# Performance work log

Measured on AMD Instinct MI355X. Metric: run time of the kernel, lower is better.

## Reference

```python
import jax, jax.numpy as jnp
import numpy as np

B, P, S, E, H, NC, NR, NL = 32, 1024, 128, 768, 8, 5, 3, 3


def _adjacency():
    adj = np.zeros((NC, NC, NR), dtype=np.float32)
    for i, j in [(0, 1), (0, 2), (1, 2), (2, 3)]:  # co-occurrence (symmetric)
        adj[i, j, 0] = 1.0
        adj[j, i, 0] = 1.0
    adj[3, 2, 1] = 1.0  # hierarchical
    for i in range(NC):  # self loops
        adj[i, i, 2] = 1.0
    return jnp.asarray(adj)


def _ln(x, g, b, eps=1e-5):
    m = x.mean(-1, keepdims=True)
    v = ((x - m) ** 2).mean(-1, keepdims=True)
    return (x - m) * jax.lax.rsqrt(v + eps) * g + b


def _mha(q, k, v, Wqkv, bqkv, Wo, bo, h=H):
    # torch nn.MultiheadAttention, batch_first=True, eval mode (no dropout),
    # returns (output, attn weights averaged over heads)
    Bq, Lq, Eq = q.shape
    Lk = k.shape[1]
    d = Eq // h
    Wq, Wk, Wv = jnp.split(Wqkv, 3, axis=0)
    bq, bk, bv = jnp.split(bqkv, 3, axis=0)
    qh = (q @ Wq.T + bq).reshape(Bq, Lq, h, d).transpose(0, 2, 1, 3)
    kh = (k @ Wk.T + bk).reshape(Bq, Lk, h, d).transpose(0, 2, 1, 3)
    vh = (v @ Wv.T + bv).reshape(Bq, Lk, h, d).transpose(0, 2, 1, 3)
    scores = jnp.einsum('bhqd,bhkd->bhqk', qh, kh) / jnp.sqrt(jnp.asarray(d, q.dtype))
    a = jax.nn.softmax(scores, axis=-1)
    o = jnp.einsum('bhqk,bhkd->bhqd', a, vh).transpose(0, 2, 1, 3).reshape(Bq, Lq, Eq)
    return o @ Wo.T + bo, a.mean(axis=1)


def setup_inputs() -> dict:
    key = jax.random.key(0)
    ks = iter(jax.random.split(key, 64))
    n = lambda *s: jax.random.normal(next(ks), s, dtype=jnp.float32) * 0.02
    return {
        'visual_features': jax.random.normal(next(ks), (B, P, E), dtype=jnp.float32),
        'text_features': jax.random.normal(next(ks), (B, S, E), dtype=jnp.float32),
        'sentence_embedding': jax.random.normal(next(ks), (B, E), dtype=jnp.float32),
        'class_presence': (jax.random.uniform(next(ks), (B, NC)) > 0.5).astype(jnp.float32),
        # graph layer params stacked over NL layers
        'g_node_emb': n(NL, NC, E), 'g_edge_emb': n(NL, NR, E),
        'g_Wqkv': n(NL, 3 * E, E), 'g_bqkv': jnp.zeros((NL, 3 * E)),
        'g_Wo': n(NL, E, E), 'g_bo': jnp.zeros((NL, E)),
        'g_W1': n(NL, E, 2 * E), 'g_b1': jnp.zeros((NL, E)),
        'g_lng': jnp.ones((NL, E)), 'g_lnb': jnp.zeros((NL, E)),
        'g_W2': n(NL, E, E), 'g_b2': jnp.zeros((NL, E)),
        # visual-text fusion MHA
        'v_Wqkv': n(3 * E, E), 'v_bqkv': jnp.zeros((3 * E,)),
        'v_Wo': n(E, E), 'v_bo': jnp.zeros((E,)),
        # per-class feature generators stacked over NC classes
        'c_W1': n(NC, E, E), 'c_b1': jnp.zeros((NC, E)),
        'c_lng': jnp.ones((NC, E)), 'c_lnb': jnp.zeros((NC, E)),
        'c_W2': n(NC, E, E), 'c_b2': jnp.zeros((NC, E)),
        # global fusion MLP
        'gf_W1': n(E, 2 * E), 'gf_b1': jnp.zeros((E,)),
        'gf_lng': jnp.ones((E,)), 'gf_lnb': jnp.zeros((E,)),
        'gf_W2': n(E, E), 'gf_b2': jnp.zeros((E,)),
        # output proj + final norm
        'out_W': n(E, E), 'out_b': jnp.zeros((E,)),
        'norm_g': jnp.ones((E,)), 'norm_b': jnp.zeros((E,)),
    }


def reference(visual_features, text_features, sentence_embedding, class_presence,
              g_node_emb, g_edge_emb, g_Wqkv, g_bqkv, g_Wo, g_bo, g_W1, g_b1,
              g_lng, g_lnb, g_W2, g_b2, v_Wqkv, v_bqkv, v_Wo, v_bo,
              c_W1, c_b1, c_lng, c_lnb, c_W2, c_b2,
              gf_W1, gf_b1, gf_lng, gf_lnb, gf_W2, gf_b2,
              out_W, out_b, norm_g, norm_b):
    adj = _adjacency()
    Bc = visual_features.shape[0]
    sent = sentence_embedding
    activated, scores = None, None
    for l in range(NL):  # small fixed layer loop
        node_emb = g_node_emb[l]  # [NC, E]
        # sum over relation types of (adj_r @ node_emb) * edge_emb_r, / NR
        edge_feat = jnp.einsum('ijr,je,re->ie', adj, node_emb, g_edge_emb[l]) / NR
        node_f = jnp.broadcast_to(node_emb, (Bc, NC, E))
        combined = jnp.concatenate([node_f, jnp.broadcast_to(edge_feat, (Bc, NC, E))], axis=-1)
        h = combined @ g_W1[l].T + g_b1[l]
        h = jax.nn.relu(_ln(h, g_lng[l], g_lnb[l]))
        updated = h @ g_W2[l].T + g_b2[l]  # [B, NC, E]
        _, w = _mha(sent[:, None, :], updated, updated, g_Wqkv[l], g_bqkv[l], g_Wo[l], g_bo[l])
        scores = jax.nn.softmax(w[:, 0, :] * (class_presence + 0.1), axis=-1)
        activated = updated * scores[..., None]
        sent = sent + activated.mean(axis=1)
    fused, _ = _mha(visual_features, text_features, text_features, v_Wqkv, v_bqkv, v_Wo, v_bo)
    grounded = _ln(visual_features + fused, norm_g, norm_b)
    # grouped per-class MLPs (batched over classes via einsum)
    cf = jnp.einsum('bce,cfe->bcf', activated, c_W1) + c_b1
    cf = jax.nn.relu(_ln(cf, c_lng, c_lnb))
    cf = jnp.einsum('bce,cfe->bcf', cf, c_W2) + c_b2
    gc = jnp.broadcast_to(sent[:, None, :], (Bc, NC, E))
    g = jnp.concatenate([cf, gc], axis=-1) @ gf_W1.T + gf_b1
    g = jax.nn.relu(_ln(g, gf_lng, gf_lnb))
    class_guidance = g @ gf_W2.T + gf_b2
    grounded_out = grounded @ out_W.T + out_b
    return grounded_out, class_guidance, scores
```

## Files before the change

kernel.cpp:

```cpp
#include <hip/hip_runtime.h>
#include <stdint.h>

typedef unsigned short u16;
typedef __attribute__((ext_vector_type(8))) short short8;
typedef __attribute__((ext_vector_type(4))) float f32x4;

#define NB 32
#define PP 1024
#define SEQ 128
#define EE 768
#define HH 8
#define DD 96
#define NCC 5
#define NLL 3

__device__ __forceinline__ float bf2f(u16 x){ unsigned u=((unsigned)x)<<16; float f; __builtin_memcpy(&f,&u,4); return f; }
__device__ __forceinline__ u16 f2bf(float f){ unsigned u; __builtin_memcpy(&u,&f,4); u=(u+0x7FFFu+((u>>16)&1u))>>16; return (u16)u; }

__device__ __forceinline__ short8 cvt8(const float* p) {
  f32x4 a = *(const f32x4*)p;
  f32x4 b = *(const f32x4*)(p+4);
  short8 r;
  r[0]=(short)f2bf(a[0]); r[1]=(short)f2bf(a[1]); r[2]=(short)f2bf(a[2]); r[3]=(short)f2bf(a[3]);
  r[4]=(short)f2bf(b[0]); r[5]=(short)f2bf(b[1]); r[6]=(short)f2bf(b[2]); r[7]=(short)f2bf(b[3]);
  return r;
}

__device__ __forceinline__ void gl16(const u16* g, u16* l) {
  __builtin_amdgcn_global_load_lds((const __attribute__((address_space(1))) void*)g,
                                   (__attribute__((address_space(3))) void*)l, 16, 0, 0);
}

__device__ __forceinline__ const u16* ah_addr(const u16* aBase, int k0) {
  const int h = k0/96;
  return aBase + (size_t)h*98304 + (k0 - h*96);
}

__global__ __launch_bounds__(256) void k_cvt4(
    const float* __restrict__ s0, u16* __restrict__ d0, int c0,
    const float* __restrict__ s1, u16* __restrict__ d1, int c1,
    const float* __restrict__ s2, u16* __restrict__ d2, int c2,
    const float* __restrict__ s3, u16* __restrict__ d3, int c3)
{
  int i = blockIdx.x*256 + threadIdx.x;
  const int stride = gridDim.x*256;
  const int tot = c0+c1+c2+c3;
  for (; i < tot; i += stride) {
    int j = i; const float* s; u16* d;
    if (j < c0) { s=s0; d=d0; }
    else { j-=c0; if (j<c1){s=s1;d=d1;}
      else { j-=c1; if (j<c2){s=s2;d=d2;} else { j-=c2; s=s3; d=d3; } } }
    *(short8*)(d + (size_t)j*8) = cvt8(s + (size_t)j*8);
  }
}

__global__ __launch_bounds__(256) void k_cvt(const float* __restrict__ s, u16* __restrict__ d, int n8) {
  int i = blockIdx.x*256 + threadIdx.x;
  const int stride = gridDim.x*256;
  for (; i < n8; i += stride) *(short8*)(d + (size_t)i*8) = cvt8(s + (size_t)i*8);
}

__device__ __forceinline__ void ln_stats(float v0, float v1, float v2, float* red, int t,
                                         float& mean, float& rstd) {
  float ps = v0+v1+v2;
  float ps2 = v0*v0+v1*v1+v2*v2;
  #pragma unroll
  for (int o=32;o;o>>=1){ ps += __shfl_down(ps,o,64); ps2 += __shfl_down(ps2,o,64); }
  if ((t&63)==0){ red[t>>6]=ps; red[4+(t>>6)]=ps2; }
  __syncthreads();
  mean = (red[0]+red[1]+red[2]+red[3])*(1.0f/EE);
  float var = (red[4]+red[5]+red[6]+red[7])*(1.0f/EE) - mean*mean;
  rstd = rsqrtf(var + 1e-5f);
  __syncthreads();
}

template<int EPI, int AH>
__global__ __launch_bounds__(256) void gemm_bt(const u16* __restrict__ A, const u16* __restrict__ Bw,
        const float* __restrict__ bias, const u16* __restrict__ Res,
        u16* __restrict__ C, float* __restrict__ Cf, u16* __restrict__ C2,
        int M, int N, int K, int NTB)
{
  __shared__ u16 As[2][4096];
  __shared__ u16 Bs[2][4096];
  const int nwg = gridDim.x;
  const int bid = blockIdx.x;
  const int task = (bid & 7)*(nwg >> 3) + (bid >> 3);
  const int m0 = (task / NTB)*128, n0 = (task % NTB)*128;
  const int t = threadIdx.x;
  const int lane = t&63, w = t>>6, wr = w>>1, wc = w&1, lm = lane&15, lg = lane>>4;
  const int o   = w*1024 + lane*16;
  const int srow = o>>6;
  const int sg   = ((o>>4)&3) ^ ((srow>>1)&3);
  const int row0 = m0 + srow;
  const u16* ag    = A + (size_t)row0*K + sg*8;
  const u16* aBase = A + (size_t)((row0>>10)*8)*98304
                       + (size_t)(row0&1023)*96 + sg*8;
  const u16* bg = Bw + (size_t)(n0+srow)*K + sg*8;
  const size_t rstepA = (size_t)64*K;
  const size_t rstepH = 6144;
  const int s  = (lm>>1)&3;
  const int ra = (wr*64+lm)*32 + (lg^s)*8;
  const int rb = (wc*64+lm)*32 + (lg^s)*8;
  const int NT = K>>5;

  f32x4 acc[4][4] = {};
  #pragma unroll
  for (int p=0;p<2;p++) {
    const int k0 = p<<5;
    if constexpr (AH) {
      const u16* pa = ah_addr(aBase, k0);
      gl16(pa,          &As[p][w*512]);
      gl16(pa + rstepH, &As[p][2048 + w*512]);
    } else {
      gl16(ag + k0,          &As[p][w*512]);
      gl16(ag + k0 + rstepA, &As[p][2048 + w*512]);
    }
    gl16(bg + k0,          &Bs[p][w*512]);
    gl16(bg + k0 + rstepA, &Bs[p][2048 + w*512]);
  }
  int cur = 0;
  for (int kt=0; kt<NT; ++kt) {
    if (kt+1 < NT) { asm volatile("s_waitcnt vmcnt(4)" ::: "memory"); }
    else           { asm volatile("s_waitcnt vmcnt(0)" ::: "memory"); }
    __builtin_amdgcn_sched_barrier(0);
    __builtin_amdgcn_s_barrier();
    short8 af[4], bf[4];
    #pragma unroll
    for (int mi=0;mi<4;mi++) af[mi] = *(const short8*)&As[cur][ra + mi*512];
    #pragma unroll
    for (int ni=0;ni<4;ni++) bf[ni] = *(const short8*)&Bs[cur][rb + ni*512];
    asm volatile("s_waitcnt lgkmcnt(0)" ::: "memory");
    __builtin_amdgcn_sched_barrier(0);
    __builtin_amdgcn_s_barrier();
    if (kt+2 < NT) {
      const int k0 = (kt+2)<<5;
      if constexpr (AH) {
        const u16* pa = ah_addr(aBase, k0);
        gl16(pa,          &As[cur][w*512]);
        gl16(pa + rstepH, &As[cur][2048 + w*512]);
      } else {
        gl16(ag + k0,          &As[cur][w*512]);
        gl16(ag + k0 + rstepA, &As[cur][2048 + w*512]);
      }
      gl16(bg + k0,          &Bs[cur][w*512]);
      gl16(bg + k0 + rstepA, &Bs[cur][2048 + w*512]);
    }
    #pragma unroll
    for (int mi=0;mi<4;mi++)
      #pragma unroll
      for (int ni=0;ni<4;ni++)
        acc[mi][ni] = __builtin_amdgcn_mfma_f32_16x16x32_bf16(af[mi], bf[ni], acc[mi][ni], 0,0,0);
    cur ^= 1;
  }
  #pragma unroll
  for (int mi=0;mi<4;mi++) {
    #pragma unroll
    for (int ni=0;ni<4;ni++) {
      const int col = n0 + wc*64 + ni*16 + lm;
      const float bv = bias[col];
      const int hq = (n0 + wc*64 + ni*16)/96;
      const int dq = col - hq*96;
      #pragma unroll
      for (int r=0;r<4;r++) {
        const int row = m0 + wr*64 + mi*16 + lg*4 + r;
        float v = acc[mi][ni][r] + bv;
        if constexpr (EPI==1) v += bf2f(Res[(size_t)row*N + col]);
        if constexpr (EPI==3) {
          Cf[(size_t)row*N + col] = v;
        } else if constexpr (EPI==2) {
          if (col < EE) C[(size_t)row*EE + col] = f2bf(v);
          else C2[((size_t)(row>>7)*EE + (col-EE))*SEQ + (row&127)] = f2bf(v);
        } else if constexpr (EPI==4) {
          C[((size_t)((row>>10)*8 + hq)*1024 + (row&1023))*96 + dq] = f2bf(v);
        } else {
          C[(size_t)row*N + col] = f2bf(v);
        }
      }
    }
  }
}

template<int MT, int AF>
__global__ __launch_bounds__(256) void gemm_tk(const void* __restrict__ Av, const float* __restrict__ W,
    float* __restrict__ Ppart, int ngroups, int KS, int K, int lda, long strideA, long strideW)
{
  const int task = blockIdx.x;
  const int nt = task % 6;
  const int g  = (task/6) % ngroups;
  const int ks = task/(6*ngroups);
  const int t = threadIdx.x, l = t&63, w = t>>6, lm = l&15, lg = l>>4;
  const int slice = K/KS, kbase = ks*slice;
  const int n0 = nt*128 + w*32;
  W += (size_t)g*strideW;
  f32x4 acc[MT/16][2] = {};
  for (int ki=0; ki<slice; ki+=32) {
    const int k0 = kbase + ki;
    short8 af[MT/16];
    #pragma unroll
    for (int m=0;m<MT/16;m++) {
      if constexpr (AF) af[m] = cvt8((const float*)Av + (size_t)g*strideA + (size_t)(m*16+lm)*lda + k0 + lg*8);
      else af[m] = *(const short8*)((const u16*)Av + (size_t)g*strideA + (size_t)(m*16+lm)*lda + k0 + lg*8);
    }
    #pragma unroll
    for (int ni=0;ni<2;ni++) {
      const short8 bf = cvt8(W + (size_t)(n0+ni*16+lm)*K + k0 + lg*8);
      #pragma unroll
      for (int m=0;m<MT/16;m++)
        acc[m][ni] = __builtin_amdgcn_mfma_f32_16x16x32_bf16(af[m], bf, acc[m][ni], 0,0,0);
    }
  }
  float* pb = Ppart + (size_t)(ks*ngroups+g)*MT*768;
  #pragma unroll
  for (int m=0;m<MT/16;m++)
    #pragma unroll
    for (int ni=0;ni<2;ni++)
      #pragma unroll
      for (int r=0;r<4;r++)
        pb[(size_t)(m*16+lg*4+r)*768 + n0+ni*16+lm] = acc[m][ni][r];
}

__global__ __launch_bounds__(256) void k_red(const float* __restrict__ Ppart,
    float* __restrict__ outF, u16* __restrict__ outB,
    const float* __restrict__ bias, long strideB,
    int MT, int ngroups, int KS, int Mreal, long strideR, long strideG)
{
  const int bid = blockIdx.x, g = bid/Mreal, rr = bid%Mreal, t = threadIdx.x;
  #pragma unroll
  for (int i=0;i<3;i++) {
    const int e = t + i*256;
    float s = bias[(size_t)g*strideB + e];
    for (int ks=0; ks<KS; ++ks) s += Ppart[((size_t)(ks*ngroups+g)*MT + rr)*768 + e];
    const size_t off = (size_t)rr*strideR + (size_t)g*strideG + e;
    if (outF) outF[off] = s;
    if (outB) outB[off] = f2bf(s);
  }
}

__global__ __launch_bounds__(256) void k_lnred(const float* __restrict__ Ppart, u16* __restrict__ out,
    const float* __restrict__ bias, long strideB,
    const float* __restrict__ gamma, const float* __restrict__ beta, long strideLn,
    int MT, int ngroups, int KS, int Mreal, long strideR, long strideG)
{
  const int bid = blockIdx.x, g = bid/Mreal, rr = bid%Mreal, t = threadIdx.x;
  __shared__ float red[8];
  float v[3];
  #pragma unroll
  for (int i=0;i<3;i++) {
    const int e = t + i*256;
    float s = bias[(size_t)g*strideB + e];
    for (int ks=0; ks<KS; ++ks) s += Ppart[((size_t)(ks*ngroups+g)*MT + rr)*768 + e];
    v[i] = s;
  }
  float mean, rstd;
  ln_stats(v[0],v[1],v[2], red, t, mean, rstd);
  #pragma unroll
  for (int i=0;i<3;i++) {
    const int e = t + i*256;
    out[(size_t)rr*strideR + (size_t)g*strideG + e] =
        f2bf(fmaxf((v[i]-mean)*rstd*gamma[(size_t)g*strideLn+e]+beta[(size_t)g*strideLn+e], 0.f));
  }
}

__global__ __launch_bounds__(256) void k_comb_si(const float* __restrict__ node_all,
    const float* __restrict__ edge_all, u16* __restrict__ comb,
    const float* __restrict__ se, float* __restrict__ sent)
{
  const int bid = blockIdx.x, t = threadIdx.x;
  if (bid < NLL*NCC) {
    const int ll = bid/NCC, c = bid%NCC;
    const float* node = node_all + (size_t)ll*NCC*EE;
    const float* edge = edge_all + (size_t)ll*3*EE;
    #pragma unroll
    for (int i=0;i<3;i++) {
      const int e = t + i*256;
      float n0=node[e], n1=node[EE+e], n2=node[2*EE+e], n3=node[3*EE+e];
      float nc_=node[(size_t)c*EE+e];
      float e0=edge[e], e1=edge[EE+e], e2=edge[2*EE+e];
      float s0;
      if (c==0) s0=n1+n2; else if (c==1) s0=n0+n2; else if (c==2) s0=n0+n1+n3; else if (c==3) s0=n2; else s0=0.f;
      float ef = (s0*e0 + ((c==3)? n2*e1 : 0.f) + nc_*e2)*(1.0f/3.0f);
      comb[(size_t)bid*2*EE + e]      = f2bf(nc_);
      comb[(size_t)bid*2*EE + EE + e] = f2bf(ef);
    }
  } else {
    const int i = (bid - NLL*NCC)*256 + t;
    if (i < NB*EE) sent[i] = se[i];
  }
}

__global__ __launch_bounds__(256) void k_attn2(int l, const float* __restrict__ qpart,
    const float* __restrict__ bq,
    const float* __restrict__ presence, const float* __restrict__ upd, const float* __restrict__ khg,
    float* __restrict__ sent, float* __restrict__ sc_ws, float* __restrict__ out_scores,
    u16* __restrict__ actB, u16* __restrict__ cat)
{
  const int b = blockIdx.x, t = threadIdx.x;
  __shared__ float qh[EE];
  __shared__ float scl[HH][NCC];
  __shared__ float wsc[NCC];
  __shared__ float scr[NCC];
  #pragma unroll
  for (int i=0;i<3;i++) {
    const int e = t + i*256;
    float s = bq[e];
    #pragma unroll
    for (int ks=0; ks<8; ++ks) s += qpart[((size_t)ks*NB + b)*768 + e];
    qh[e] = s;
  }
  __syncthreads();
  if (t < HH*NCC) {
    const int hh=t/NCC, cc=t%NCC;
    const float* kr = khg + (size_t)(l*NCC+cc)*EE + hh*DD;
    float a=0.f;
    #pragma unroll 8
    for (int d=0;d<DD;d++) a += qh[hh*DD+d]*kr[d];
    scl[hh][cc]=a*0.1020620726159658f;
  }
  __syncthreads();
  if (t < HH) {
    float m=scl[t][0];
    #pragma unroll
    for (int c2=1;c2<NCC;c2++) m=fmaxf(m,scl[t][c2]);
    float ex[NCC]; float s=0.f;
    #pragma unroll
    for (int c2=0;c2<NCC;c2++){ ex[c2]=__expf(scl[t][c2]-m); s+=ex[c2]; }
    #pragma unroll
    for (int c2=0;c2<NCC;c2++) scl[t][c2]=ex[c2]/s;
  }
  __syncthreads();
  if (t < NCC) {
    float wv=0.f;
    #pragma unroll
    for (int hh=0;hh<HH;hh++) wv += scl[hh][t];
    wv *= (1.0f/HH);
    wsc[t] = wv*(presence[b*NCC+t]+0.1f);
  }
  __syncthreads();
  if (t==0) {
    float m=wsc[0];
    #pragma unroll
    for (int c2=1;c2<NCC;c2++) m=fmaxf(m,wsc[c2]);
    float ex[NCC]; float s=0.f;
    #pragma unroll
    for (int c2=0;c2<NCC;c2++){ ex[c2]=__expf(wsc[c2]-m); s+=ex[c2]; }
    #pragma unroll
    for (int c2=0;c2<NCC;c2++){
      float v=ex[c2]/s; scr[c2]=v; sc_ws[b*NCC+c2]=v;
      if (out_scores) out_scores[b*NCC+c2]=v;
    }
  }
  __syncthreads();
  #pragma unroll
  for (int i=0;i<3;i++) {
    const int e=t+i*256;
    float a=0.f;
    #pragma unroll
    for (int c2=0;c2<NCC;c2++) a += scr[c2]*upd[(size_t)(l*NCC+c2)*EE+e];
    const float sn = sent[(size_t)b*EE+e] + a*(1.0f/NCC);
    sent[(size_t)b*EE+e] = sn;
    if (out_scores) {
      const u16 snb = f2bf(sn);
      #pragma unroll
      for (int c2=0;c2<NCC;c2++) {
        actB[((size_t)c2*NB + b)*EE + e] = f2bf(upd[(size_t)(2*NCC+c2)*EE + e]*scr[c2]);
        cat[((size_t)(b*NCC+c2))*2*EE + EE + e] = snb;
      }
    }
  }
}

__global__ __launch_bounds__(256) void attn_k(u16* __restrict__ Q, const u16* __restrict__ Kb,
                                              const u16* __restrict__ Vt)
{
  const int qs = blockIdx.x, h = blockIdx.y, b = blockIdx.z;
  const int t = threadIdx.x, l = t&63, w = t>>6, wr = w>>1, wc = w&1, lm = l&15, lg = l>>4;
  __shared__ u16 Ps[64][136];
  __shared__ float reds[2][64];
  const u16* kb = Kb + ((size_t)b*SEQ)*EE + h*DD;
  const u16* vb = Vt + ((size_t)(b*HH+h))*DD*SEQ;
  u16* qbase = Q + ((size_t)(b*HH+h)*PP + (size_t)qs*512)*DD;
  const float scale = 0.1020620726159658f;

  short8 bv[3][4], vv[4][3];
  #pragma unroll
  for (int kc=0;kc<3;kc++)
    #pragma unroll
    for (int ni=0;ni<4;ni++)
      bv[kc][ni] = *(const short8*)(kb + (size_t)(wc*64+ni*16+lm)*EE + kc*32 + lg*8);
  #pragma unroll
  for (int kc=0;kc<4;kc++)
    #pragma unroll
    for (int ni=0;ni<3;ni++)
      vv[kc][ni] = *(const short8*)(vb + (size_t)(wc*48+ni*16+lm)*SEQ + kc*32 + lg*8);

  short8 af[3][2];
  #pragma unroll
  for (int kc=0;kc<3;kc++)
    #pragma unroll
    for (int mi=0;mi<2;mi++)
      af[kc][mi] = *(const short8*)(qbase + (size_t)(wr*32+mi*16+lm)*DD + kc*32 + lg*8);

  for (int it=0; it<8; ++it) {
    u16* qb = qbase + (size_t)it*64*DD;
    f32x4 acc[2][4] = {};
    #pragma unroll
    for (int kc=0;kc<3;kc++)
      #pragma unroll
      for (int mi=0;mi<2;mi++)
        #pragma unroll
        for (int ni=0;ni<4;ni++)
          acc[mi][ni] = __builtin_amdgcn_mfma_f32_16x16x32_bf16(af[kc][mi], bv[kc][ni], acc[mi][ni], 0,0,0);
    if (it < 7) {
      const u16* qn = qb + (size_t)64*DD;
      #pragma unroll
      for (int kc=0;kc<3;kc++)
        #pragma unroll
        for (int mi=0;mi<2;mi++)
          af[kc][mi] = *(const short8*)(qn + (size_t)(wr*32+mi*16+lm)*DD + kc*32 + lg*8);
    }
    float gsum[2][4];
    #pragma unroll
    for (int mi=0;mi<2;mi++)
      #pragma unroll
      for (int r=0;r<4;r++) {
        float s=0.f;
        #pragma unroll
        for (int ni=0;ni<4;ni++) {
          float p = __expf(acc[mi][ni][r]*scale);
          acc[mi][ni][r]=p; s+=p;
        }
        #pragma unroll
        for (int mk=1;mk<16;mk<<=1) s += __shfl_xor(s,mk,64);
        gsum[mi][r]=s;
      }
    if (lm==0) {
      #pragma unroll
      for (int mi=0;mi<2;mi++)
        #pragma unroll
        for (int r=0;r<4;r++) reds[wc][wr*32+mi*16+lg*4+r] = gsum[mi][r];
    }
    __syncthreads();
    #pragma unroll
    for (int mi=0;mi<2;mi++)
      #pragma unroll
      for (int r=0;r<4;r++) {
        const int row = wr*32+mi*16+lg*4+r;
        const float inv = 1.0f/(reds[0][row]+reds[1][row]);
        #pragma unroll
        for (int ni=0;ni<4;ni++)
          Ps[row][wc*64+ni*16+lm] = f2bf(acc[mi][ni][r]*inv);
      }
    __syncthreads();

    f32x4 oacc[2][3] = {};
    #pragma unroll
    for (int kc=0;kc<4;kc++) {
      short8 pa[2];
      #pragma unroll
      for (int mi=0;mi<2;mi++) pa[mi] = *(const short8*)&Ps[wr*32+mi*16+lm][kc*32+lg*8];
      #pragma unroll
      for (int mi=0;mi<2;mi++)
        #pragma unroll
        for (int ni=0;ni<3;ni++)
          oacc[mi][ni] = __builtin_amdgcn_mfma_f32_16x16x32_bf16(pa[mi], vv[kc][ni], oacc[mi][ni], 0,0,0);
    }
    #pragma unroll
    for (int mi=0;mi<2;mi++)
      #pragma unroll
      for (int ni=0;ni<3;ni++)
        #pragma unroll
        for (int r=0;r<4;r++)
          qb[(size_t)(wr*32+mi*16+lg*4+r)*DD + wc*48+ni*16+lm] = f2bf(oacc[mi][ni][r]);
    __syncthreads();
  }
}

__global__ __launch_bounds__(256) void k_ln(u16* __restrict__ G, const float* __restrict__ gw, const float* __restrict__ gb)
{
  const int row = blockIdx.x, t = threadIdx.x;
  u16* p = G + (size_t)row*EE;
  __shared__ float red[8];
  float v[3];
  #pragma unroll
  for (int i=0;i<3;i++) v[i]=bf2f(p[t+i*256]);
  float mean, rstd;
  ln_stats(v[0],v[1],v[2], red, t, mean, rstd);
  #pragma unroll
  for (int i=0;i<3;i++) {
    const int e=t+i*256;
    p[e]=f2bf((v[i]-mean)*rstd*gw[e]+gb[e]);
  }
}

extern "C" void kernel_launch(void* const* d_in, const int* in_sizes, int n_in,
                              void* d_out, int out_size, void* d_ws, size_t ws_size,
                              hipStream_t stream)
{
  const float* visual   = (const float*)d_in[0];
  const float* text     = (const float*)d_in[1];
  const float* sentemb  = (const float*)d_in[2];
  const float* presence = (const float*)d_in[3];
  const float* gnode = (const float*)d_in[4];
  const float* gedge = (const float*)d_in[5];
  const float* gWqkv = (const float*)d_in[6];
  const float* gbqkv = (const float*)d_in[7];
  const float* gW1 = (const float*)d_in[10];
  const float* gb1 = (const float*)d_in[11];
  const float* glng = (const float*)d_in[12];
  const float* glnb = (const float*)d_in[13];
  const float* gW2 = (const float*)d_in[14];
  const float* gb2 = (const float*)d_in[15];
  const float* vWqkv = (const float*)d_in[16];
  const float* vbqkv = (const float*)d_in[17];
  const float* vWo = (const float*)d_in[18];
  const float* vbo = (const float*)d_in[19];
  const float* cW1 = (const float*)d_in[20];
  const float* cb1 = (const float*)d_in[21];
  const float* clng = (const float*)d_in[22];
  const float* clnb = (const float*)d_in[23];
  const float* cW2 = (const float*)d_in[24];
  const float* cb2 = (const float*)d_in[25];
  const float* gfW1 = (const float*)d_in[26];
  const float* gfb1 = (const float*)d_in[27];
  const float* gflng = (const float*)d_in[28];
  const float* gflnb = (const float*)d_in[29];
  const float* gfW2 = (const float*)d_in[30];
  const float* gfb2 = (const float*)d_in[31];
  const float* outW = (const float*)d_in[32];
  const float* outb = (const float*)d_in[33];
  const float* normg = (const float*)d_in[34];
  const float* normb = (const float*)d_in[35];

  char* ws = (char*)d_ws;
  u16* wsG   = (u16*)(ws);
  u16* wsK   = (u16*)(ws + 50331648);
  u16* wsVt  = (u16*)(ws + 56623104);
  u16* visB  = (u16*)(ws + 62914560);
  u16* outWB = wsK;

  char* dob = (char*)d_out;
  u16* wsQ    = (u16*)(dob);
  u16* textB  = (u16*)(dob + 50331648);
  u16* WqkvB  = (u16*)(dob + 56623104);
  u16* WoB    = (u16*)(dob + 60162048);
  char* P = dob + 61341696;
  float* wsSent   = (float*)(P);
  float* wsUpd    = (float*)(P +   98304);
  float* wsKhg    = (float*)(P +  144384);
  float* wsScores = (float*)(P +  190464);
  u16*   wsComb   = (u16*)  (P +  191104);
  u16*   wsHb     = (u16*)  (P +  237184);
  u16*   wsUpdB   = (u16*)  (P +  260224);
  u16*   wsActB   = (u16*)  (P +  283264);
  u16*   wsH1b    = (u16*)  (P +  529024);
  u16*   wsCat    = (u16*)  (P +  774784);
  u16*   wsG1b    = (u16*)  (P + 1266304);
  float* Ppart    = (float*)(P + 1512064);

  float* outGO = (float*)d_out;
  float* outCG = outGO + 25165824;
  float* outSC = outGO + 25288704;

  k_cvt4<<<dim3(2048), dim3(256), 0, stream>>>(visual, visB, 3145728,
                                               text, textB, 393216,
                                               vWqkv, WqkvB, 221184,
                                               vWo, WoB, 73728);

  k_comb_si<<<dim3(NLL*NCC + 96), dim3(256), 0, stream>>>(gnode, gedge, wsComb, sentemb, wsSent);
  gemm_tk<16,0><<<dim3(144), dim3(256), 0, stream>>>(wsComb, gW1, Ppart,
      3, 8, 2*EE, 2*EE, (long)NCC*2*EE, (long)EE*2*EE);
  k_lnred<<<dim3(15), dim3(256), 0, stream>>>(Ppart, wsHb, gb1, EE, glng, glnb, EE,
      16, 3, 8, 5, 768, 3840);
  gemm_tk<16,0><<<dim3(72), dim3(256), 0, stream>>>(wsHb, gW2, Ppart,
      3, 4, EE, EE, (long)NCC*EE, (long)EE*EE);
  k_red<<<dim3(15), dim3(256), 0, stream>>>(Ppart, wsUpd, wsUpdB, gb2, EE,
      16, 3, 4, 5, 768, 3840);
  gemm_tk<16,0><<<dim3(72), dim3(256), 0, stream>>>(wsUpdB, gWqkv + (size_t)EE*EE, Ppart,
      3, 4, EE, EE, (long)NCC*EE, (long)3*EE*EE);
  k_red<<<dim3(15), dim3(256), 0, stream>>>(Ppart, wsKhg, nullptr, gbqkv + EE, (long)3*EE,
      16, 3, 4, 5, 768, 3840);

  for (int l=0;l<NLL;l++) {
    gemm_tk<32,1><<<dim3(48), dim3(256), 0, stream>>>(wsSent, gWqkv + (size_t)l*3*EE*EE, Ppart,
        1, 8, EE, EE, 0, 0);
    k_attn2<<<dim3(NB), dim3(256), 0, stream>>>(l, Ppart, gbqkv + (size_t)l*3*EE,
        presence, wsUpd, wsKhg, wsSent, wsScores,
        (l==NLL-1)?outSC:(float*)nullptr, wsActB, wsCat);
  }

  gemm_tk<32,0><<<dim3(120), dim3(256), 0, stream>>>(wsActB, cW1, Ppart,
      5, 4, EE, EE, (long)NB*EE, (long)EE*EE);
  k_lnred<<<dim3(160), dim3(256), 0, stream>>>(Ppart, wsH1b, cb1, EE, clng, clnb, EE,
      32, 5, 4, 32, 768, 24576);
  gemm_tk<32,0><<<dim3(120), dim3(256), 0, stream>>>(wsH1b, cW2, Ppart,
      5, 4, EE, EE, (long)NB*EE, (long)EE*EE);
  k_red<<<dim3(160), dim3(256), 0, stream>>>(Ppart, nullptr, wsCat, cb2, EE,
      32, 5, 4, 32, 7680, 1536);
  gemm_tk<32,0><<<dim3(120), dim3(256), 0, stream>>>(wsCat, gfW1, Ppart,
      5, 4, 2*EE, 2*EE, (long)NB*2*EE, 0);
  k_lnred<<<dim3(160), dim3(256), 0, stream>>>(Ppart, wsG1b, gfb1, 0, gflng, gflnb, 0,
      32, 5, 4, 32, 768, 24576);
  gemm_tk<32,0><<<dim3(120), dim3(256), 0, stream>>>(wsG1b, gfW2, Ppart,
      5, 4, EE, EE, (long)NB*EE, 0);
  k_red<<<dim3(160), dim3(256), 0, stream>>>(Ppart, outCG, nullptr, gfb2, 0,
      32, 5, 4, 32, 768, 24576);

  gemm_bt<4,0><<<dim3(1536), dim3(256), 0, stream>>>(visB, WqkvB, vbqkv, nullptr,
                                                     wsQ, nullptr, nullptr, NB*PP, EE, EE, 6);
  gemm_bt<2,0><<<dim3(384), dim3(256), 0, stream>>>(textB, WqkvB + (size_t)EE*EE, vbqkv+EE, nullptr,
                                                    wsK, nullptr, wsVt, NB*SEQ, 2*EE, EE, 12);
  attn_k<<<dim3(2, HH, NB), dim3(256), 0, stream>>>(wsQ, wsK, wsVt);
  k_cvt<<<dim3(512), dim3(256), 0, stream>>>(outW, outWB, 73728);
  gemm_bt<1,1><<<dim3(1536), dim3(256), 0, stream>>>(wsQ, WoB, vbo, visB,
                                                     wsG, nullptr, nullptr, NB*PP, EE, EE, 6);
  k_ln<<<dim3(NB*PP), dim3(256), 0, stream>>>(wsG, normg, normb);
  gemm_bt<3,0><<<dim3(1536), dim3(256), 0, stream>>>(wsG, outWB, outb, nullptr,
                                                     nullptr, outGO, nullptr, NB*PP, EE, EE, 6);
}
```

Measured before the change: 432.9 us.

## Enlarge GEMM tile to 256x128 with each wave owning full N width

The bf16 MFMA GEMM tile grows from 128x128 to 256x128 rows per workgroup. Each of the four waves now computes 64 rows by all 128 columns (4x8 MFMA accumulators), and grid sizes are halved to match. This raises arithmetic intensity per loaded B tile and cuts the number of workgroups. In exchange it doubles accumulator registers and A-tile LDS, which may lower occupancy, and with only 768 blocks per large GEMM the tail-wave balance on the device changes.

```diff
diff --git a/kernel.cpp b/kernel.cpp
--- a/kernel.cpp
+++ b/kernel.cpp
@@ -80,14 +80,14 @@
         u16* __restrict__ C, float* __restrict__ Cf, u16* __restrict__ C2,
         int M, int N, int K, int NTB)
 {
-  __shared__ u16 As[2][4096];
+  __shared__ u16 As[2][8192];
   __shared__ u16 Bs[2][4096];
   const int nwg = gridDim.x;
   const int bid = blockIdx.x;
   const int task = (bid & 7)*(nwg >> 3) + (bid >> 3);
-  const int m0 = (task / NTB)*128, n0 = (task % NTB)*128;
+  const int m0 = (task / NTB)*256, n0 = (task % NTB)*128;
   const int t = threadIdx.x;
-  const int lane = t&63, w = t>>6, wr = w>>1, wc = w&1, lm = lane&15, lg = lane>>4;
+  const int lane = t&63, w = t>>6, lm = lane&15, lg = lane>>4;
   const int o   = w*1024 + lane*16;
   const int srow = o>>6;
   const int sg   = ((o>>4)&3) ^ ((srow>>1)&3);
@@ -99,36 +99,36 @@
   const size_t rstepA = (size_t)64*K;
   const size_t rstepH = 6144;
   const int s  = (lm>>1)&3;
-  const int ra = (wr*64+lm)*32 + (lg^s)*8;
-  const int rb = (wc*64+lm)*32 + (lg^s)*8;
+  const int ra = (w*64+lm)*32 + (lg^s)*8;
+  const int rb = lm*32 + (lg^s)*8;
   const int NT = K>>5;
 
-  f32x4 acc[4][4] = {};
+  f32x4 acc[4][8] = {};
   #pragma unroll
   for (int p=0;p<2;p++) {
     const int k0 = p<<5;
     if constexpr (AH) {
       const u16* pa = ah_addr(aBase, k0);
-      gl16(pa,          &As[p][w*512]);
-      gl16(pa + rstepH, &As[p][2048 + w*512]);
+      #pragma unroll
+      for (int c=0;c<4;c++) gl16(pa + (size_t)c*rstepH, &As[p][c*2048 + w*512]);
     } else {
-      gl16(ag + k0,          &As[p][w*512]);
-      gl16(ag + k0 + rstepA, &As[p][2048 + w*512]);
-    }
-    gl16(bg + k0,          &Bs[p][w*512]);
-    gl16(bg + k0 + rstepA, &Bs[p][2048 + w*512]);
+      #pragma unroll
+      for (int c=0;c<4;c++) gl16(ag + k0 + (size_t)c*rstepA, &As[p][c*2048 + w*512]);
+    }
+    #pragma unroll
+    for (int c=0;c<2;c++) gl16(bg + k0 + (size_t)c*rstepA, &Bs[p][c*2048 + w*512]);
   }
   int cur = 0;
   for (int kt=0; kt<NT; ++kt) {
-    if (kt+1 < NT) { asm volatile("s_waitcnt vmcnt(4)" ::: "memory"); }
+    if (kt+1 < NT) { asm volatile("s_waitcnt vmcnt(6)" ::: "memory"); }
     else           { asm volatile("s_waitcnt vmcnt(0)" ::: "memory"); }
     __builtin_amdgcn_sched_barrier(0);
     __builtin_amdgcn_s_barrier();
-    short8 af[4], bf[4];
+    short8 af[4], bf[8];
     #pragma unroll
     for (int mi=0;mi<4;mi++) af[mi] = *(const short8*)&As[cur][ra + mi*512];
     #pragma unroll
-    for (int ni=0;ni<4;ni++) bf[ni] = *(const short8*)&Bs[cur][rb + ni*512];
+    for (int ni=0;ni<8;ni++) bf[ni] = *(const short8*)&Bs[cur][rb + ni*512];
     asm volatile("s_waitcnt lgkmcnt(0)" ::: "memory");
     __builtin_amdgcn_sched_barrier(0);
     __builtin_amdgcn_s_barrier();
@@ -136,33 +136,33 @@
       const int k0 = (kt+2)<<5;
       if constexpr (AH) {
         const u16* pa = ah_addr(aBase, k0);
-        gl16(pa,          &As[cur][w*512]);
-        gl16(pa + rstepH, &As[cur][2048 + w*512]);
+        #pragma unroll
+        for (int c=0;c<4;c++) gl16(pa + (size_t)c*rstepH, &As[cur][c*2048 + w*512]);
       } else {
-        gl16(ag + k0,          &As[cur][w*512]);
-        gl16(ag + k0 + rstepA, &As[cur][2048 + w*512]);
+        #pragma unroll
+        for (int c=0;c<4;c++) gl16(ag + k0 + (size_t)c*rstepA, &As[cur][c*2048 + w*512]);
       }
-      gl16(bg + k0,          &Bs[cur][w*512]);
-      gl16(bg + k0 + rstepA, &Bs[cur][2048 + w*512]);
+      #pragma unroll
+      for (int c=0;c<2;c++) gl16(bg + k0 + (size_t)c*rstepA, &Bs[cur][c*2048 + w*512]);
     }
     #pragma unroll
     for (int mi=0;mi<4;mi++)
       #pragma unroll
-      for (int ni=0;ni<4;ni++)
+      for (int ni=0;ni<8;ni++)
         acc[mi][ni] = __builtin_amdgcn_mfma_f32_16x16x32_bf16(af[mi], bf[ni], acc[mi][ni], 0,0,0);
     cur ^= 1;
   }
   #pragma unroll
   for (int mi=0;mi<4;mi++) {
     #pragma unroll
-    for (int ni=0;ni<4;ni++) {
-      const int col = n0 + wc*64 + ni*16 + lm;
+    for (int ni=0;ni<8;ni++) {
+      const int col = n0 + ni*16 + lm;
       const float bv = bias[col];
-      const int hq = (n0 + wc*64 + ni*16)/96;
+      const int hq = (n0 + ni*16)/96;
       const int dq = col - hq*96;
       #pragma unroll
       for (int r=0;r<4;r++) {
-        const int row = m0 + wr*64 + mi*16 + lg*4 + r;
+        const int row = m0 + w*64 + mi*16 + lg*4 + r;
         float v = acc[mi][ni][r] + bv;
         if constexpr (EPI==1) v += bf2f(Res[(size_t)row*N + col]);
         if constexpr (EPI==3) {
@@ -605,15 +605,15 @@
   k_red<<<dim3(160), dim3(256), 0, stream>>>(Ppart, outCG, nullptr, gfb2, 0,
       32, 5, 4, 32, 768, 24576);
 
-  gemm_bt<4,0><<<dim3(1536), dim3(256), 0, stream>>>(visB, WqkvB, vbqkv, nullptr,
-                                                     wsQ, nullptr, nullptr, NB*PP, EE, EE, 6);
-  gemm_bt<2,0><<<dim3(384), dim3(256), 0, stream>>>(textB, WqkvB + (size_t)EE*EE, vbqkv+EE, nullptr,
+  gemm_bt<4,0><<<dim3(768), dim3(256), 0, stream>>>(visB, WqkvB, vbqkv, nullptr,
+                                                    wsQ, nullptr, nullptr, NB*PP, EE, EE, 6);
+  gemm_bt<2,0><<<dim3(192), dim3(256), 0, stream>>>(textB, WqkvB + (size_t)EE*EE, vbqkv+EE, nullptr,
                                                     wsK, nullptr, wsVt, NB*SEQ, 2*EE, EE, 12);
   attn_k<<<dim3(2, HH, NB), dim3(256), 0, stream>>>(wsQ, wsK, wsVt);
   k_cvt<<<dim3(512), dim3(256), 0, stream>>>(outW, outWB, 73728);
-  gemm_bt<1,1><<<dim3(1536), dim3(256), 0, stream>>>(wsQ, WoB, vbo, visB,
-                                                     wsG, nullptr, nullptr, NB*PP, EE, EE, 6);
+  gemm_bt<1,1><<<dim3(768), dim3(256), 0, stream>>>(wsQ, WoB, vbo, visB,
+                                                    wsG, nullptr, nullptr, NB*PP, EE, EE, 6);
   k_ln<<<dim3(NB*PP), dim3(256), 0, stream>>>(wsG, normg, normb);
-  gemm_bt<3,0><<<dim3(1536), dim3(256), 0, stream>>>(wsG, outWB, outb, nullptr,
-                                                     nullptr, outGO, nullptr, NB*PP, EE, EE, 6);
-}
+  gemm_bt<3,0><<<dim3(768), dim3(256), 0, stream>>>(wsG, outWB, outb, nullptr,
+                                                    nullptr, outGO, nullptr, NB*PP, EE, EE, 6);
+}
```

After: 477.2 us. 10.2% more time.

## Use 256x256-tile 512-thread GEMM kernel for the large visual projections

Applied to the files above, without the earlier changes.

Adds a gemm_bt8 kernel that computes 256x256 output tiles with 8 waves, where half the waves load A and half load B into double-buffered LDS. Each wave holds an 8x4 MFMA accumulator block. The three large M=32768 GEMMs (Q projection, output projection with residual, final output linear) now use it with 384 blocks instead of 1536 128x128 tiles. This raises data reuse per LDS load, in exchange for higher register pressure, 64KB of LDS per block, and fewer blocks to fill the CUs. The old kernel drops its unused epilogue and head-layout paths.

```diff
diff --git a/kernel.cpp b/kernel.cpp
--- a/kernel.cpp
+++ b/kernel.cpp
@@ -72,6 +72,117 @@
   float var = (red[4]+red[5]+red[6]+red[7])*(1.0f/EE) - mean*mean;
   rstd = rsqrtf(var + 1e-5f);
   __syncthreads();
+}
+
+template<int EPI, int AH>
+__global__ __launch_bounds__(512, 2) void gemm_bt8(const u16* __restrict__ A, const u16* __restrict__ Bw,
+        const float* __restrict__ bias, const u16* __restrict__ Res,
+        u16* __restrict__ C, float* __restrict__ Cf,
+        int M, int N, int K, int NTB)
+{
+  __shared__ u16 As[2][8192];
+  __shared__ u16 Bs[2][8192];
+  const int nwg = gridDim.x;
+  const int bid = blockIdx.x;
+  const int task = (bid & 7)*(nwg >> 3) + (bid >> 3);
+  const int m0 = (task / NTB)*256, n0 = (task % NTB)*256;
+  const int t = threadIdx.x;
+  const int lane = t&63, w = t>>6;
+  const int wm = w>>2, wn = w&3, lm = lane&15, lg = lane>>4;
+  const int wg = w&3;
+  const int o   = wg*1024 + lane*16;
+  const int srow = o>>6;
+  const int sg   = ((o>>4)&3) ^ ((srow>>1)&3);
+  const int arow0 = m0 + srow;
+  const u16* ag    = A + (size_t)arow0*K + sg*8;
+  const u16* aBase = A + (size_t)((arow0>>10)*8)*98304
+                       + (size_t)(arow0&1023)*96 + sg*8;
+  const u16* bg = Bw + (size_t)(n0+srow)*K + sg*8;
+  const size_t rstepA = (size_t)64*K;
+  const size_t rstepH = 6144;
+  const int s  = (lm>>1)&3;
+  const int ra = (wm*128 + lm)*32 + (lg^s)*8;
+  const int rb = (wn*64  + lm)*32 + (lg^s)*8;
+  const int NT = K>>5;
+
+  f32x4 acc[8][4] = {};
+  #pragma unroll
+  for (int p=0;p<2;p++) {
+    const int k0 = p<<5;
+    if (wm==0) {
+      if constexpr (AH) {
+        const u16* pa = ah_addr(aBase, k0);
+        #pragma unroll
+        for (int c=0;c<4;c++) gl16(pa + (size_t)c*rstepH, &As[p][c*2048 + wg*512]);
+      } else {
+        #pragma unroll
+        for (int c=0;c<4;c++) gl16(ag + k0 + (size_t)c*rstepA, &As[p][c*2048 + wg*512]);
+      }
+    } else {
+      #pragma unroll
+      for (int c=0;c<4;c++) gl16(bg + k0 + (size_t)c*rstepA, &Bs[p][c*2048 + wg*512]);
+    }
+  }
+  int cur = 0;
+  for (int kt=0; kt<NT; ++kt) {
+    if (kt+1 < NT) { asm volatile("s_waitcnt vmcnt(4)" ::: "memory"); }
+    else           { asm volatile("s_waitcnt vmcnt(0)" ::: "memory"); }
+    __builtin_amdgcn_sched_barrier(0);
+    __builtin_amdgcn_s_barrier();
+    short8 af[8], bf[4];
+    #pragma unroll
+    for (int mi=0;mi<8;mi++) af[mi] = *(const short8*)&As[cur][ra + mi*512];
+    #pragma unroll
+    for (int ni=0;ni<4;ni++) bf[ni] = *(const short8*)&Bs[cur][rb + ni*512];
+    asm volatile("s_waitcnt lgkmcnt(0)" ::: "memory");
+    __builtin_amdgcn_sched_barrier(0);
+    __builtin_amdgcn_s_barrier();
+    if (kt+2 < NT) {
+      const int k0 = (kt+2)<<5;
+      if (wm==0) {
+        if constexpr (AH) {
+          const u16* pa = ah_addr(aBase, k0);
+          #pragma unroll
+          for (int c=0;c<4;c++) gl16(pa + (size_t)c*rstepH, &As[cur][c*2048 + wg*512]);
+        } else {
+          #pragma unroll
+          for (int c=0;c<4;c++) gl16(ag + k0 + (size_t)c*rstepA, &As[cur][c*2048 + wg*512]);
+        }
+      } else {
+        #pragma unroll
+        for (int c=0;c<4;c++) gl16(bg + k0 + (size_t)c*rstepA, &Bs[cur][c*2048 + wg*512]);
+      }
+    }
+    #pragma unroll
+    for (int mi=0;mi<8;mi++)
+      #pragma unroll
+      for (int ni=0;ni<4;ni++)
+        acc[mi][ni] = __builtin_amdgcn_mfma_f32_16x16x32_bf16(af[mi], bf[ni], acc[mi][ni], 0,0,0);
+    cur ^= 1;
+  }
+  #pragma unroll
+  for (int mi=0;mi<8;mi++) {
+    #pragma unroll
+    for (int ni=0;ni<4;ni++) {
+      const int col = n0 + wn*64 + ni*16 + lm;
+      const float bv = bias[col];
+      const int hq = (n0 + wn*64 + ni*16)/96;
+      const int dq = col - hq*96;
+      #pragma unroll
+      for (int r=0;r<4;r++) {
+        const int row = m0 + wm*128 + mi*16 + lg*4 + r;
+        float v = acc[mi][ni][r] + bv;
+        if constexpr (EPI==1) v += bf2f(Res[(size_t)row*N + col]);
+        if constexpr (EPI==3) {
+          Cf[(size_t)row*N + col] = v;
+        } else if constexpr (EPI==4) {
+          C[((size_t)((row>>10)*8 + hq)*1024 + (row&1023))*96 + dq] = f2bf(v);
+        } else {
+          C[(size_t)row*N + col] = f2bf(v);
+        }
+      }
+    }
+  }
 }
 
 template<int EPI, int AH>
@@ -93,11 +204,8 @@
   const int sg   = ((o>>4)&3) ^ ((srow>>1)&3);
   const int row0 = m0 + srow;
   const u16* ag    = A + (size_t)row0*K + sg*8;
-  const u16* aBase = A + (size_t)((row0>>10)*8)*98304
-                       + (size_t)(row0&1023)*96 + sg*8;
   const u16* bg = Bw + (size_t)(n0+srow)*K + sg*8;
   const size_t rstepA = (size_t)64*K;
-  const size_t rstepH = 6144;
   const int s  = (lm>>1)&3;
   const int ra = (wr*64+lm)*32 + (lg^s)*8;
   const int rb = (wc*64+lm)*32 + (lg^s)*8;
@@ -107,14 +215,8 @@
   #pragma unroll
   for (int p=0;p<2;p++) {
     const int k0 = p<<5;
-    if constexpr (AH) {
-      const u16* pa = ah_addr(aBase, k0);
-      gl16(pa,          &As[p][w*512]);
-      gl16(pa + rstepH, &As[p][2048 + w*512]);
-    } else {
-      gl16(ag + k0,          &As[p][w*512]);
-      gl16(ag + k0 + rstepA, &As[p][2048 + w*512]);
-    }
+    gl16(ag + k0,          &As[p][w*512]);
+    gl16(ag + k0 + rstepA, &As[p][2048 + w*512]);
     gl16(bg + k0,          &Bs[p][w*512]);
     gl16(bg + k0 + rstepA, &Bs[p][2048 + w*512]);
   }
@@ -134,14 +236,8 @@
     __builtin_amdgcn_s_barrier();
     if (kt+2 < NT) {
       const int k0 = (kt+2)<<5;
-      if constexpr (AH) {
-        const u16* pa = ah_addr(aBase, k0);
-        gl16(pa,          &As[cur][w*512]);
-        gl16(pa + rstepH, &As[cur][2048 + w*512]);
-      } else {
-        gl16(ag + k0,          &As[cur][w*512]);
-        gl16(ag + k0 + rstepA, &As[cur][2048 + w*512]);
-      }
+      gl16(ag + k0,          &As[cur][w*512]);
+      gl16(ag + k0 + rstepA, &As[cur][2048 + w*512]);
       gl16(bg + k0,          &Bs[cur][w*512]);
       gl16(bg + k0 + rstepA, &Bs[cur][2048 + w*512]);
     }
@@ -158,20 +254,13 @@
     for (int ni=0;ni<4;ni++) {
       const int col = n0 + wc*64 + ni*16 + lm;
       const float bv = bias[col];
-      const int hq = (n0 + wc*64 + ni*16)/96;
-      const int dq = col - hq*96;
       #pragma unroll
       for (int r=0;r<4;r++) {
         const int row = m0 + wr*64 + mi*16 + lg*4 + r;
         float v = acc[mi][ni][r] + bv;
-        if constexpr (EPI==1) v += bf2f(Res[(size_t)row*N + col]);
-        if constexpr (EPI==3) {
-          Cf[(size_t)row*N + col] = v;
-        } else if constexpr (EPI==2) {
+        if constexpr (EPI==2) {
           if (col < EE) C[(size_t)row*EE + col] = f2bf(v);
           else C2[((size_t)(row>>7)*EE + (col-EE))*SEQ + (row&127)] = f2bf(v);
-        } else if constexpr (EPI==4) {
-          C[((size_t)((row>>10)*8 + hq)*1024 + (row&1023))*96 + dq] = f2bf(v);
         } else {
           C[(size_t)row*N + col] = f2bf(v);
         }
@@ -605,15 +694,15 @@
   k_red<<<dim3(160), dim3(256), 0, stream>>>(Ppart, outCG, nullptr, gfb2, 0,
       32, 5, 4, 32, 768, 24576);
 
-  gemm_bt<4,0><<<dim3(1536), dim3(256), 0, stream>>>(visB, WqkvB, vbqkv, nullptr,
-                                                     wsQ, nullptr, nullptr, NB*PP, EE, EE, 6);
+  gemm_bt8<4,0><<<dim3(384), dim3(512), 0, stream>>>(visB, WqkvB, vbqkv, nullptr,
+                                                     wsQ, nullptr, NB*PP, EE, EE, 3);
   gemm_bt<2,0><<<dim3(384), dim3(256), 0, stream>>>(textB, WqkvB + (size_t)EE*EE, vbqkv+EE, nullptr,
                                                     wsK, nullptr, wsVt, NB*SEQ, 2*EE, EE, 12);
   attn_k<<<dim3(2, HH, NB), dim3(256), 0, stream>>>(wsQ, wsK, wsVt);
   k_cvt<<<dim3(512), dim3(256), 0, stream>>>(outW, outWB, 73728);
-  gemm_bt<1,1><<<dim3(1536), dim3(256), 0, stream>>>(wsQ, WoB, vbo, visB,
-                                                     wsG, nullptr, nullptr, NB*PP, EE, EE, 6);
+  gemm_bt8<1,1><<<dim3(384), dim3(512), 0, stream>>>(wsQ, WoB, vbo, visB,
+                                                     wsG, nullptr, NB*PP, EE, EE, 3);
   k_ln<<<dim3(NB*PP), dim3(256), 0, stream>>>(wsG, normg, normb);
-  gemm_bt<3,0><<<dim3(1536), dim3(256), 0, stream>>>(wsG, outWB, outb, nullptr,
-                                                     nullptr, outGO, nullptr, NB*PP, EE, EE, 6);
-}
+  gemm_bt8<3,0><<<dim3(384), dim3(512), 0, stream>>>(wsG, outWB, outb, nullptr,
+                                                     nullptr, outGO, NB*PP, EE, EE, 3);
+}
```

New measurement: 454.0 us. +4.9%, slower.
